# Optimization experiments

Hardware: AMD Instinct MI355X
Metric: run time of the kernel (lower is better)

The kernel has to match this reference:

```python
import jax, jax.numpy as jnp
import numpy as np

MIN_SPAN = 3
MAX_SPAN = 20
LEN_BONUS = 0.01
LN_EPS = 1e-5


def setup_inputs() -> dict:
    key = jax.random.key(0)
    ks = jax.random.split(key, 10)
    B, S, H = 16, 2048, 1024
    D = H // 2
    hidden_states = jax.random.normal(ks[0], (B, S, H), dtype=jnp.float32)
    lengths = jax.random.randint(ks[1], (B,), S // 2, S + 1)
    attention_mask = (jnp.arange(S)[None, :] < lengths[:, None]).astype(jnp.int32)
    return {
        'hidden_states': hidden_states,
        'attention_mask': attention_mask,
        'Wq': 0.02 * jax.random.normal(ks[2], (H, D), dtype=jnp.float32),
        'bq': jnp.zeros((D,), jnp.float32),
        'Wk': 0.02 * jax.random.normal(ks[3], (H, D), dtype=jnp.float32),
        'bk': jnp.zeros((D,), jnp.float32),
        'W1': 0.02 * jax.random.normal(ks[4], (H, D), dtype=jnp.float32),
        'b1': jnp.zeros((D,), jnp.float32),
        'ln_g': jnp.ones((D,), jnp.float32),
        'ln_b': jnp.zeros((D,), jnp.float32),
        'W2': 0.01 * jax.random.normal(ks[5], (D, 1), dtype=jnp.float32),
        'b2': jnp.zeros((1,), jnp.float32),
    }


def _token_scores(hidden_states, mask, Wq, bq, Wk, bk, W1, b1, ln_g, ln_b, W2, b2):
    q = hidden_states @ Wq + bq                      # [B,S,D]
    k = hidden_states @ Wk + bk                      # [B,S,D]
    d = q.shape[-1]
    scores = jnp.einsum('bsd,btd->bst', q, k) / jnp.sqrt(jnp.float32(d))
    scores = jnp.where(mask[:, None, :], scores, -10000.0)
    probs = jax.nn.softmax(scores, axis=-1)
    context = jnp.einsum('bst,bth->bsh', probs, hidden_states)  # [B,S,H]
    h = context @ W1 + b1
    mu = jnp.mean(h, axis=-1, keepdims=True)
    var = jnp.var(h, axis=-1, keepdims=True)
    h = (h - mu) * jax.lax.rsqrt(var + LN_EPS) * ln_g + ln_b
    h = jax.nn.relu(h)                               # dropout: eval mode -> identity
    ts = (h @ W2 + b2)[..., 0]                       # [B,S]
    return jnp.where(mask, ts, -10000.0)


def _rationale_mask(token_scores, mask):
    # Faithful to original: starts[0]==0 always, so prefix subtraction never
    # fires; span score = cumsum[start+L-1]/L + bonus. Argmax over (L asc, start asc)
    # with strict-greater updates == first max of the flattened (L, start) grid.
    B, S = token_scores.shape
    valid_len = jnp.sum(mask, axis=1)                # [B] int
    cum = jnp.cumsum(token_scores, axis=1)           # [B,S]
    L = jnp.arange(MIN_SPAN, MAX_SPAN + 1)           # [NL]
    starts = jnp.arange(S)                           # [S]
    end = jnp.clip(starts[None, :] + L[:, None] - 1, 0, S - 1)   # [NL,S]
    bonus = LEN_BONUS * (L.astype(jnp.float32) / MAX_SPAN)       # [NL]
    grid = cum[:, end] / L[None, :, None].astype(jnp.float32) + bonus[None, :, None]  # [B,NL,S]
    vl = valid_len[:, None, None]
    valid = (L[None, :, None] <= vl) & (starts[None, None, :] <= vl - L[None, :, None])
    grid = jnp.where(valid, grid, -jnp.inf)
    idx = jnp.argmax(grid.reshape(B, -1), axis=1)    # first max -> torch tie-break
    best_L = MIN_SPAN + idx // S
    best_s = idx % S
    pos = jnp.arange(S)[None, :]
    span = (pos >= best_s[:, None]) & (pos < (best_s + best_L)[:, None])
    short = (valid_len <= MIN_SPAN)[:, None]
    short_span = pos < valid_len[:, None]
    return jnp.where(short, short_span, span).astype(token_scores.dtype)


def reference(hidden_states, attention_mask, Wq, bq, Wk, bk, W1, b1, ln_g, ln_b, W2, b2):
    mask = attention_mask.astype(bool)
    token_scores = _token_scores(hidden_states, mask, Wq, bq, Wk, bk, W1, b1, ln_g, ln_b, W2, b2)
    rationale = _rationale_mask(token_scores, mask)
    token_probs = jax.nn.softmax(jnp.where(mask, token_scores, -10000.0), axis=-1)
    attended = hidden_states * rationale[:, :, None]
    lengths = jnp.sum(rationale, axis=1, keepdims=True) + 1e-6
    pooled = jnp.sum(attended, axis=1) / lengths
    return token_scores, rationale, token_probs, attended, pooled
```

## Files before the change

kernel.cpp:

```cpp
#include <hip/hip_runtime.h>

typedef _Float16 f16;
typedef __attribute__((ext_vector_type(8))) _Float16 f16x8;
typedef __attribute__((ext_vector_type(4))) _Float16 f16x4v;
typedef __attribute__((ext_vector_type(4))) float f32x4;

#define B_ 16
#define S_ 2048
#define H_ 1024
#define D_ 512

__device__ __forceinline__ void gload16(const f16* g, f16* l) {
  __builtin_amdgcn_global_load_lds(
      (const __attribute__((address_space(1))) unsigned int*)g,
      (__attribute__((address_space(3))) unsigned int*)l, 16, 0, 0);
}

__global__ __launch_bounds__(256) void cvt_hs_kernel(const float4* __restrict__ in,
                                                     f16x4v* __restrict__ out) {
  long long i = (long long)blockIdx.x * 256 + threadIdx.x;
  float4 v = in[i];
  f16x4v o = {(f16)v.x, (f16)v.y, (f16)v.z, (f16)v.w};
  out[i] = o;
}

__global__ __launch_bounds__(256) void setup_kernel(
    const float* __restrict__ Wq, const float* __restrict__ Wk,
    const float* __restrict__ W1, const float* __restrict__ bq,
    const float* __restrict__ bk, const float* __restrict__ b1,
    const int* __restrict__ mask, f16* __restrict__ Wt,
    float* __restrict__ bias, int* __restrict__ lens) {
  const int blk = blockIdx.x;
  const int tid = threadIdx.x;
  if (blk < 6144) {
    int i = blk * 256 + tid;
    int n = i >> 10;
    int k = i & 1023;
    const float* src = (n < 512) ? Wq : ((n < 1024) ? Wk : W1);
    Wt[i] = (f16)src[k * 512 + (n & 511)];
  } else if (blk < 6150) {
    int i = (blk - 6144) * 256 + tid;
    if (i < 1536) bias[i] = (i < 512) ? bq[i] : ((i < 1024) ? bk[i - 512] : b1[i - 1024]);
  } else {
    int b = blk - 6150;
    int s = 0;
    for (int c = tid; c < S_; c += 256) s += mask[b * S_ + c];
    __shared__ int r[256];
    r[tid] = s;
    __syncthreads();
    for (int o = 128; o > 0; o >>= 1) {
      if (tid < o) r[tid] += r[tid + o];
      __syncthreads();
    }
    if (tid == 0) lens[b] = r[0];
  }
}

template <int MW>
__global__ __launch_bounds__(256, MW) void gemm_bt(
    const f16* __restrict__ A, const f16* __restrict__ Bm, void* __restrict__ Cout,
    void* __restrict__ Cout2,
    int K, int lda, int ldb, int ldc,
    long long sA, long long sB, long long sC,
    float scale, const float* __restrict__ bias, int mode,
    const int* __restrict__ lens, int lflags, int mgrp) {
  const int bz = blockIdx.z;

  const int ntiles = gridDim.x, mtiles = gridDim.y;
  const int flat = blockIdx.y * ntiles + blockIdx.x;
  const int per = mgrp * ntiles;
  const int grp = flat / per;
  const int rem = flat - grp * per;
  const int gbase = grp * mgrp;
  int gsz = mtiles - gbase;
  if (gsz > mgrp) gsz = mgrp;
  const int mt = gbase + rem % gsz;
  const int nt = rem / gsz;
  const int m0 = mt * 128;
  const int n0 = nt * 128;

  int Keff = K;
  if (lflags) {
    const int len = lens[(lflags & 1) ? (m0 >> 11) : bz];
    if ((lflags & 3) && (m0 & 2047) >= len) return;
    if ((lflags & 4) && n0 >= len) return;
    if (lflags & 8) { int kl = (len + 63) & ~63; Keff = kl < K ? kl : K; }
  }

  A += (long long)bz * sA;
  Bm += (long long)bz * sB;

  __shared__ f16 As[128 * 64];
  __shared__ f16 Bs[128 * 64];

  const int tid = threadIdx.x;
  const int lane = tid & 63;
  const int wid = tid >> 6;
  const int wm = wid & 1, wn = wid >> 1;

  f32x4 acc[4][4] = {};

  const int lr8 = lane >> 3;
  const int sg = lane & 7;

  for (int k0 = 0; k0 < Keff; k0 += 64) {
#pragma unroll
    for (int it = 0; it < 4; ++it) {
      const int r0 = it * 32 + wid * 8;
      const int r = r0 + lr8;
      const int cg = sg ^ (r & 7);
      gload16(A + (long long)(m0 + r) * lda + k0 + cg * 8, As + r0 * 64);
      gload16(Bm + (long long)(n0 + r) * ldb + k0 + cg * 8, Bs + r0 * 64);
    }
    __syncthreads();

#pragma unroll
    for (int kk = 0; kk < 64; kk += 32) {
      const int cg = (kk >> 3) + (lane >> 4);
      f16x8 af[4], bf[4];
#pragma unroll
      for (int i = 0; i < 4; ++i) {
        const int row = wm * 64 + i * 16 + (lane & 15);
        af[i] = *(const f16x8*)(As + row * 64 + ((cg ^ (row & 7)) << 3));
      }
#pragma unroll
      for (int j = 0; j < 4; ++j) {
        const int row = wn * 64 + j * 16 + (lane & 15);
        bf[j] = *(const f16x8*)(Bs + row * 64 + ((cg ^ (row & 7)) << 3));
      }
#pragma unroll
      for (int i = 0; i < 4; ++i)
#pragma unroll
        for (int j = 0; j < 4; ++j)
          acc[i][j] = __builtin_amdgcn_mfma_f32_16x16x32_f16(af[i], bf[j], acc[i][j], 0, 0, 0);
    }
    __syncthreads();
  }

  const long long cb = (long long)bz * sC;
  const int lr = ((lane >> 4) << 2);
  const int lc = lane & 15;
#pragma unroll
  for (int i = 0; i < 4; ++i) {
#pragma unroll
    for (int j = 0; j < 4; ++j) {
      const int col = n0 + wn * 64 + j * 16 + lc;
      const float bv = bias ? bias[col] : 0.0f;
      if (mode == 2 || (mode == 3 && col >= 1024)) {
        const int rowb = m0 + wm * 64 + i * 16 + lr;
        const int b = rowb >> 11, t = rowb & 2047;
        const int d = (mode == 3) ? (col - 1024) : col;
        f16* dst = (f16*)((mode == 3) ? Cout2 : Cout);
        f16x4v pk;
#pragma unroll
        for (int r = 0; r < 4; ++r) pk[r] = (f16)(acc[i][j][r] * scale + bv);
        *(f16x4v*)(dst + ((long long)b << 20) + (long long)d * 2048 + t) = pk;
      } else {
#pragma unroll
        for (int r = 0; r < 4; ++r) {
          const int row = m0 + wm * 64 + i * 16 + lr + r;
          float v = acc[i][j][r] * scale + bv;
          if (mode == 0)
            ((float*)Cout)[cb + (long long)row * ldc + col] = v;
          else
            ((f16*)Cout)[cb + (long long)row * ldc + col] = (f16)v;
        }
      }
    }
  }
}

__global__ __launch_bounds__(256) void softmax_rows_kernel(f16* __restrict__ sc,
                                                           const int* __restrict__ lens) {
  const int tid = threadIdx.x;
  const int lane = tid & 63;
  const int row = blockIdx.x * 4 + (tid >> 6);
  const int len = lens[row >> 11];
  const int cl = (len + 127) & ~127;
  if ((row & 2047) >= cl) return;
  f16* p = sc + (long long)row * S_;

  f16x8 v[4];
#pragma unroll
  for (int c = 0; c < 4; ++c)
    if (c * 512 < cl) v[c] = *(const f16x8*)(p + c * 512 + lane * 8);

  float m = -1e30f;
#pragma unroll
  for (int c = 0; c < 4; ++c) {
    if (c * 512 >= cl) continue;
#pragma unroll
    for (int j = 0; j < 8; ++j) {
      const int col = c * 512 + lane * 8 + j;
      if (col < len) m = fmaxf(m, (float)v[c][j]);
    }
  }
#pragma unroll
  for (int o = 32; o > 0; o >>= 1) m = fmaxf(m, __shfl_xor(m, o, 64));

  float e[32];
  float s = 0.0f;
#pragma unroll
  for (int c = 0; c < 4; ++c) {
    if (c * 512 >= cl) continue;
#pragma unroll
    for (int j = 0; j < 8; ++j) {
      const int col = c * 512 + lane * 8 + j;
      const float x = (col < len) ? __expf((float)v[c][j] - m) : 0.0f;
      e[c * 8 + j] = x;
      s += x;
    }
  }
#pragma unroll
  for (int o = 32; o > 0; o >>= 1) s += __shfl_xor(s, o, 64);
  const float inv = 1.0f / s;

#pragma unroll
  for (int c = 0; c < 4; ++c) {
    if (c * 512 >= cl) continue;
    f16x8 w;
#pragma unroll
    for (int j = 0; j < 8; ++j) w[j] = (f16)(e[c * 8 + j] * inv);
    *(f16x8*)(p + c * 512 + lane * 8) = w;
  }
}

__global__ __launch_bounds__(256) void ln_score_kernel(
    const float* __restrict__ h, const int* __restrict__ lens,
    const float* __restrict__ g, const float* __restrict__ bt,
    const float* __restrict__ W2, const float* __restrict__ b2,
    float* __restrict__ ts, float* __restrict__ out_ts) {
  const int token = blockIdx.x;
  const int tid = threadIdx.x;
  const int b = token >> 11, s = token & (S_ - 1);
  if (s >= lens[b]) {
    if (tid == 0) { ts[token] = -10000.0f; out_ts[token] = -10000.0f; }
    return;
  }
  const float* hp = h + (long long)token * D_;
  float x0 = hp[tid], x1 = hp[tid + 256];
  __shared__ float r1[256], r2[256];
  r1[tid] = x0 + x1;
  r2[tid] = x0 * x0 + x1 * x1;
  __syncthreads();
  for (int o = 128; o > 0; o >>= 1) {
    if (tid < o) { r1[tid] += r1[tid + o]; r2[tid] += r2[tid + o]; }
    __syncthreads();
  }
  const float mu = r1[0] * (1.0f / D_);
  const float var = r2[0] * (1.0f / D_) - mu * mu;
  const float rs = rsqrtf(var + 1e-5f);
  float y0 = fmaxf((x0 - mu) * rs * g[tid] + bt[tid], 0.0f);
  float y1 = fmaxf((x1 - mu) * rs * g[tid + 256] + bt[tid + 256], 0.0f);
  float d = y0 * W2[tid] + y1 * W2[tid + 256];
  __syncthreads();
  r1[tid] = d;
  __syncthreads();
  for (int o = 128; o > 0; o >>= 1) {
    if (tid < o) r1[tid] += r1[tid + o];
    __syncthreads();
  }
  if (tid == 0) {
    float v = r1[0] + b2[0];
    ts[token] = v;
    out_ts[token] = v;
  }
}

__global__ __launch_bounds__(256) void rationale_kernel(
    const float* __restrict__ ts, const int* __restrict__ lens,
    float* __restrict__ out_rat, int* __restrict__ span) {
  const int b = blockIdx.x;
  const int tid = threadIdx.x;
  const int len = lens[b];
  __shared__ float cum[S_];
  __shared__ float rbest[256];
  __shared__ int ridx[256];

  for (int s = tid; s < S_; s += 256)
    cum[s] = (s < len) ? ts[b * S_ + s] : -10000.0f;
  __syncthreads();
  if (tid == 0) {
    float a = 0.0f;
    for (int s = 0; s < S_; s += 4) {
      float4 v = *(float4*)(cum + s);
      a += v.x; v.x = a;
      a += v.y; v.y = a;
      a += v.z; v.z = a;
      a += v.w; v.w = a;
      *(float4*)(cum + s) = v;
    }
  }
  __syncthreads();

  float best = -3.4e38f;
  int bidx = 0x7fffffff;
  for (int idx = tid; idx < 18 * S_; idx += 256) {
    const int l = idx >> 11;
    const int s = idx & (S_ - 1);
    const int L = l + 3;
    if (L <= len && s <= len - L) {
      const float gv = cum[s + L - 1] / (float)L + 0.01f * ((float)L / 20.0f);
      if (gv > best) { best = gv; bidx = idx; }
    }
  }
  rbest[tid] = best;
  ridx[tid] = bidx;
  __syncthreads();
  for (int o = 128; o > 0; o >>= 1) {
    if (tid < o) {
      if (rbest[tid + o] > rbest[tid] ||
          (rbest[tid + o] == rbest[tid] && ridx[tid + o] < ridx[tid])) {
        rbest[tid] = rbest[tid + o];
        ridx[tid] = ridx[tid + o];
      }
    }
    __syncthreads();
  }
  const int bi = ridx[0];
  int start, sl;
  if (len <= 3) { start = 0; sl = len; }
  else { start = bi & (S_ - 1); sl = (bi >> 11) + 3; }
  if (tid == 0) { span[2 * b] = start; span[2 * b + 1] = sl; }
  for (int s = tid; s < S_; s += 256)
    out_rat[b * S_ + s] = (s >= start && s < start + sl) ? 1.0f : 0.0f;
}

__global__ __launch_bounds__(256) void tprobs_kernel(const float* __restrict__ ts,
                                                     const int* __restrict__ lens,
                                                     float* __restrict__ out) {
  const int b = blockIdx.x;
  const int tid = threadIdx.x;
  const int len = lens[b];
  const float* p = ts + b * S_;
  __shared__ float r[256];
  float m = -1e30f;
  for (int c = tid; c < len; c += 256) m = fmaxf(m, p[c]);
  r[tid] = m;
  __syncthreads();
  for (int o = 128; o > 0; o >>= 1) {
    if (tid < o) r[tid] = fmaxf(r[tid], r[tid + o]);
    __syncthreads();
  }
  m = r[0];
  __syncthreads();
  float s = 0.0f;
  for (int c = tid; c < len; c += 256) s += expf(p[c] - m);
  r[tid] = s;
  __syncthreads();
  for (int o = 128; o > 0; o >>= 1) {
    if (tid < o) r[tid] += r[tid + o];
    __syncthreads();
  }
  const float inv = 1.0f / r[0];
  for (int c = tid; c < S_; c += 256)
    out[b * S_ + c] = (c < len) ? expf(p[c] - m) * inv : 0.0f;
}

__global__ __launch_bounds__(256) void attended_kernel(const float4* __restrict__ hs,
                                                       const int* __restrict__ span,
                                                       float4* __restrict__ out) {
  long long i = (long long)blockIdx.x * 256 + threadIdx.x;
  const int token = (int)(i >> 8);
  const int b = token >> 11;
  const int s = token & (S_ - 1);
  const int st = span[2 * b], ln = span[2 * b + 1];
  float4 v = {0.0f, 0.0f, 0.0f, 0.0f};
  if (s >= st && s < st + ln) v = hs[i];
  out[i] = v;
}

__global__ __launch_bounds__(256) void pooled_kernel(const float* __restrict__ hs,
                                                     const int* __restrict__ span,
                                                     float* __restrict__ out) {
  const int b = blockIdx.x;
  const int tid = threadIdx.x;
  const int st = span[2 * b], ln = span[2 * b + 1];
  const float inv = 1.0f / ((float)ln + 1e-6f);
  for (int h = tid; h < H_; h += 256) {
    float s = 0.0f;
    for (int t = st; t < st + ln; ++t)
      s += hs[(long long)(b * S_ + t) * H_ + h];
    out[b * H_ + h] = s * inv;
  }
}

extern "C" void kernel_launch(void* const* d_in, const int* in_sizes, int n_in,
                              void* d_out, int out_size, void* d_ws, size_t ws_size,
                              hipStream_t stream) {
  const float* hs = (const float*)d_in[0];
  const int* amask = (const int*)d_in[1];
  const float* Wq = (const float*)d_in[2];
  const float* bq = (const float*)d_in[3];
  const float* Wk = (const float*)d_in[4];
  const float* bk = (const float*)d_in[5];
  const float* W1 = (const float*)d_in[6];
  const float* b1 = (const float*)d_in[7];
  const float* ln_g = (const float*)d_in[8];
  const float* ln_b = (const float*)d_in[9];
  const float* W2 = (const float*)d_in[10];
  const float* b2 = (const float*)d_in[11];

  float* out = (float*)d_out;
  char* ws = (char*)d_ws;

  const long long off_hs16 = 0;
  const long long off_qk = 67108864;
  const long long off_vt = 134217728;
  const long long off_wt = 167772160;
  const long long off_bias = 170917888;
  const long long off_ts = 170926080;
  const long long off_lens = 171057152;
  const long long off_span = 171057216;
  const long long off_scores = 171057408;

  f16* hs16 = (f16*)(ws + off_hs16);
  float* hbuf = (float*)(ws + off_hs16);
  f16* qk16 = (f16*)(ws + off_qk);
  f16* vt = (f16*)(ws + off_vt);
  f16* Wt = (f16*)(ws + off_wt);
  float* bias_full = (float*)(ws + off_bias);
  float* ts = (float*)(ws + off_ts);
  int* lens = (int*)(ws + off_lens);
  int* span = (int*)(ws + off_span);
  f16* scores = (f16*)(ws + off_scores);

  const long long SC_PER_B = (long long)S_ * S_ * 2;
  int nb = 16;
  while (nb > 1 && off_scores + (long long)nb * SC_PER_B > (long long)ws_size) nb >>= 1;

  float* out_ts = out;
  float* out_rat = out + 32768;
  float* out_tp = out + 65536;
  float4* out_att = (float4*)(out + 98304);
  float* out_pool = out + 33652736;

  setup_kernel<<<dim3(6166), dim3(256), 0, stream>>>(Wq, Wk, W1, bq, bk, b1, amask,
                                                     Wt, bias_full, lens);
  cvt_hs_kernel<<<dim3(32768), dim3(256), 0, stream>>>((const float4*)hs, (f16x4v*)hs16);

  gemm_bt<2><<<dim3(12, 256, 1), dim3(256), 0, stream>>>(
      hs16, Wt, (void*)qk16, (void*)vt, 1024, 1024, 1024, 1024,
      0LL, 0LL, 0LL, 1.0f, bias_full, 3, lens, 1, 8);

  const int chunks = 16 / nb;
  for (int c = 0; c < chunks; ++c) {
    const int b0 = c * nb;
    gemm_bt<4><<<dim3(16, 16, nb), dim3(256), 0, stream>>>(
        qk16 + (long long)b0 * S_ * 1024,
        qk16 + (long long)b0 * S_ * 1024 + 512,
        (void*)scores, (void*)nullptr, 512, 1024, 1024, 2048,
        (long long)S_ * 1024, (long long)S_ * 1024, (long long)S_ * S_,
        0.044194173824159216f , (const float*)nullptr, 1,
        lens + b0, 2 | 4, 8);
    softmax_rows_kernel<<<dim3(nb * S_ / 4), dim3(256), 0, stream>>>(scores, lens + b0);
    gemm_bt<4><<<dim3(4, 16, nb), dim3(256), 0, stream>>>(
        scores, vt + ((long long)b0 << 20),
        (void*)(hbuf + (long long)b0 * S_ * D_), (void*)nullptr, 2048, 2048, 2048, 512,
        (long long)S_ * S_, 1LL << 20, (long long)S_ * D_,
        1.0f, (const float*)nullptr, 0, lens + b0, 2 | 8, 1);
  }

  ln_score_kernel<<<dim3(B_ * S_), dim3(256), 0, stream>>>(hbuf, lens, ln_g, ln_b,
                                                           W2, b2, ts, out_ts);
  rationale_kernel<<<dim3(B_), dim3(256), 0, stream>>>(ts, lens, out_rat, span);
  tprobs_kernel<<<dim3(B_), dim3(256), 0, stream>>>(ts, lens, out_tp);
  attended_kernel<<<dim3(32768), dim3(256), 0, stream>>>((const float4*)hs, span, out_att);
  pooled_kernel<<<dim3(B_), dim3(256), 0, stream>>>(hs, span, out_pool);
}
```

Measured before the change: 667.6 us.

## Merge setup/convert, tail kernels; warp-per-token layernorm; skip masked token conversion

Fuses the fp16 conversion of hidden states into the setup kernel and skips converting tokens whose mask is zero. Rewrites the layernorm-score kernel so one 64-lane wavefront handles one token, using vector loads and shuffle reductions in place of shared-memory tree reductions. Also merges the rationale and token-probability kernels, and the attended and pooled kernels, to cut launch count. Skipping masked tokens leaves their fp16 rows uninitialised, which relies on downstream GEMMs ignoring rows past each sequence length.

```diff
diff --git a/kernel.cpp b/kernel.cpp
--- a/kernel.cpp
+++ b/kernel.cpp
@@ -16,33 +16,32 @@
       (__attribute__((address_space(3))) unsigned int*)l, 16, 0, 0);
 }
 
-__global__ __launch_bounds__(256) void cvt_hs_kernel(const float4* __restrict__ in,
-                                                     f16x4v* __restrict__ out) {
-  long long i = (long long)blockIdx.x * 256 + threadIdx.x;
-  float4 v = in[i];
-  f16x4v o = {(f16)v.x, (f16)v.y, (f16)v.z, (f16)v.w};
-  out[i] = o;
-}
-
-__global__ __launch_bounds__(256) void setup_kernel(
+__global__ __launch_bounds__(256) void setup_cvt_kernel(
+    const float4* __restrict__ hs4, const int* __restrict__ mask,
     const float* __restrict__ Wq, const float* __restrict__ Wk,
     const float* __restrict__ W1, const float* __restrict__ bq,
     const float* __restrict__ bk, const float* __restrict__ b1,
-    const int* __restrict__ mask, f16* __restrict__ Wt,
+    f16x4v* __restrict__ hs16, f16* __restrict__ Wt,
     float* __restrict__ bias, int* __restrict__ lens) {
   const int blk = blockIdx.x;
   const int tid = threadIdx.x;
-  if (blk < 6144) {
-    int i = blk * 256 + tid;
+  if (blk < 32768) {
+    if (mask[blk] == 0) return;
+    long long i = (long long)blk * 256 + tid;
+    float4 v = hs4[i];
+    f16x4v o = {(f16)v.x, (f16)v.y, (f16)v.z, (f16)v.w};
+    hs16[i] = o;
+  } else if (blk < 32768 + 6144) {
+    int i = (blk - 32768) * 256 + tid;
     int n = i >> 10;
     int k = i & 1023;
     const float* src = (n < 512) ? Wq : ((n < 1024) ? Wk : W1);
     Wt[i] = (f16)src[k * 512 + (n & 511)];
-  } else if (blk < 6150) {
-    int i = (blk - 6144) * 256 + tid;
+  } else if (blk < 32768 + 6150) {
+    int i = (blk - 32768 - 6144) * 256 + tid;
     if (i < 1536) bias[i] = (i < 512) ? bq[i] : ((i < 1024) ? bk[i - 512] : b1[i - 1024]);
   } else {
-    int b = blk - 6150;
+    int b = blk - 32768 - 6150;
     int s = 0;
     for (int c = tid; c < S_; c += 256) s += mask[b * S_ + c];
     __shared__ int r[256];
@@ -230,46 +229,54 @@
     const float* __restrict__ g, const float* __restrict__ bt,
     const float* __restrict__ W2, const float* __restrict__ b2,
     float* __restrict__ ts, float* __restrict__ out_ts) {
-  const int token = blockIdx.x;
-  const int tid = threadIdx.x;
+  const int tid = threadIdx.x;
+  const int lane = tid & 63;
+  const int token = blockIdx.x * 4 + (tid >> 6);
   const int b = token >> 11, s = token & (S_ - 1);
   if (s >= lens[b]) {
-    if (tid == 0) { ts[token] = -10000.0f; out_ts[token] = -10000.0f; }
+    if (lane == 0) { ts[token] = -10000.0f; out_ts[token] = -10000.0f; }
     return;
   }
   const float* hp = h + (long long)token * D_;
-  float x0 = hp[tid], x1 = hp[tid + 256];
-  __shared__ float r1[256], r2[256];
-  r1[tid] = x0 + x1;
-  r2[tid] = x0 * x0 + x1 * x1;
-  __syncthreads();
-  for (int o = 128; o > 0; o >>= 1) {
-    if (tid < o) { r1[tid] += r1[tid + o]; r2[tid] += r2[tid + o]; }
-    __syncthreads();
-  }
-  const float mu = r1[0] * (1.0f / D_);
-  const float var = r2[0] * (1.0f / D_) - mu * mu;
+  const int o8 = lane * 8;
+  float4 xa = *(const float4*)(hp + o8);
+  float4 xb = *(const float4*)(hp + o8 + 4);
+  float s1 = xa.x + xa.y + xa.z + xa.w + xb.x + xb.y + xb.z + xb.w;
+  float s2 = xa.x * xa.x + xa.y * xa.y + xa.z * xa.z + xa.w * xa.w +
+             xb.x * xb.x + xb.y * xb.y + xb.z * xb.z + xb.w * xb.w;
+#pragma unroll
+  for (int o = 32; o > 0; o >>= 1) {
+    s1 += __shfl_xor(s1, o, 64);
+    s2 += __shfl_xor(s2, o, 64);
+  }
+  const float mu = s1 * (1.0f / D_);
+  const float var = s2 * (1.0f / D_) - mu * mu;
   const float rs = rsqrtf(var + 1e-5f);
-  float y0 = fmaxf((x0 - mu) * rs * g[tid] + bt[tid], 0.0f);
-  float y1 = fmaxf((x1 - mu) * rs * g[tid + 256] + bt[tid + 256], 0.0f);
-  float d = y0 * W2[tid] + y1 * W2[tid + 256];
-  __syncthreads();
-  r1[tid] = d;
-  __syncthreads();
-  for (int o = 128; o > 0; o >>= 1) {
-    if (tid < o) r1[tid] += r1[tid + o];
-    __syncthreads();
-  }
-  if (tid == 0) {
-    float v = r1[0] + b2[0];
+  float4 ga = *(const float4*)(g + o8), gb = *(const float4*)(g + o8 + 4);
+  float4 ba = *(const float4*)(bt + o8), bb = *(const float4*)(bt + o8 + 4);
+  float4 wa = *(const float4*)(W2 + o8), wb = *(const float4*)(W2 + o8 + 4);
+  float d = 0.0f;
+  d += fmaxf((xa.x - mu) * rs * ga.x + ba.x, 0.0f) * wa.x;
+  d += fmaxf((xa.y - mu) * rs * ga.y + ba.y, 0.0f) * wa.y;
+  d += fmaxf((xa.z - mu) * rs * ga.z + ba.z, 0.0f) * wa.z;
+  d += fmaxf((xa.w - mu) * rs * ga.w + ba.w, 0.0f) * wa.w;
+  d += fmaxf((xb.x - mu) * rs * gb.x + bb.x, 0.0f) * wb.x;
+  d += fmaxf((xb.y - mu) * rs * gb.y + bb.y, 0.0f) * wb.y;
+  d += fmaxf((xb.z - mu) * rs * gb.z + bb.z, 0.0f) * wb.z;
+  d += fmaxf((xb.w - mu) * rs * gb.w + bb.w, 0.0f) * wb.w;
+#pragma unroll
+  for (int o = 32; o > 0; o >>= 1) d += __shfl_xor(d, o, 64);
+  if (lane == 0) {
+    float v = d + b2[0];
     ts[token] = v;
     out_ts[token] = v;
   }
 }
 
-__global__ __launch_bounds__(256) void rationale_kernel(
+__global__ __launch_bounds__(256) void rat_tprobs_kernel(
     const float* __restrict__ ts, const int* __restrict__ lens,
-    float* __restrict__ out_rat, int* __restrict__ span) {
+    float* __restrict__ out_rat, float* __restrict__ out_tp,
+    int* __restrict__ span) {
   const int b = blockIdx.x;
   const int tid = threadIdx.x;
   const int len = lens[b];
@@ -324,64 +331,57 @@
   if (tid == 0) { span[2 * b] = start; span[2 * b + 1] = sl; }
   for (int s = tid; s < S_; s += 256)
     out_rat[b * S_ + s] = (s >= start && s < start + sl) ? 1.0f : 0.0f;
-}
-
-__global__ __launch_bounds__(256) void tprobs_kernel(const float* __restrict__ ts,
-                                                     const int* __restrict__ lens,
-                                                     float* __restrict__ out) {
-  const int b = blockIdx.x;
-  const int tid = threadIdx.x;
-  const int len = lens[b];
+
+  __syncthreads();
   const float* p = ts + b * S_;
-  __shared__ float r[256];
   float m = -1e30f;
   for (int c = tid; c < len; c += 256) m = fmaxf(m, p[c]);
-  r[tid] = m;
+  rbest[tid] = m;
   __syncthreads();
   for (int o = 128; o > 0; o >>= 1) {
-    if (tid < o) r[tid] = fmaxf(r[tid], r[tid + o]);
-    __syncthreads();
-  }
-  m = r[0];
-  __syncthreads();
-  float s = 0.0f;
-  for (int c = tid; c < len; c += 256) s += expf(p[c] - m);
-  r[tid] = s;
+    if (tid < o) rbest[tid] = fmaxf(rbest[tid], rbest[tid + o]);
+    __syncthreads();
+  }
+  m = rbest[0];
+  __syncthreads();
+  float sm = 0.0f;
+  for (int c = tid; c < len; c += 256) sm += expf(p[c] - m);
+  rbest[tid] = sm;
   __syncthreads();
   for (int o = 128; o > 0; o >>= 1) {
-    if (tid < o) r[tid] += r[tid + o];
-    __syncthreads();
-  }
-  const float inv = 1.0f / r[0];
+    if (tid < o) rbest[tid] += rbest[tid + o];
+    __syncthreads();
+  }
+  const float inv = 1.0f / rbest[0];
   for (int c = tid; c < S_; c += 256)
-    out[b * S_ + c] = (c < len) ? expf(p[c] - m) * inv : 0.0f;
-}
-
-__global__ __launch_bounds__(256) void attended_kernel(const float4* __restrict__ hs,
-                                                       const int* __restrict__ span,
-                                                       float4* __restrict__ out) {
-  long long i = (long long)blockIdx.x * 256 + threadIdx.x;
-  const int token = (int)(i >> 8);
-  const int b = token >> 11;
-  const int s = token & (S_ - 1);
-  const int st = span[2 * b], ln = span[2 * b + 1];
-  float4 v = {0.0f, 0.0f, 0.0f, 0.0f};
-  if (s >= st && s < st + ln) v = hs[i];
-  out[i] = v;
-}
-
-__global__ __launch_bounds__(256) void pooled_kernel(const float* __restrict__ hs,
-                                                     const int* __restrict__ span,
-                                                     float* __restrict__ out) {
-  const int b = blockIdx.x;
-  const int tid = threadIdx.x;
-  const int st = span[2 * b], ln = span[2 * b + 1];
-  const float inv = 1.0f / ((float)ln + 1e-6f);
-  for (int h = tid; h < H_; h += 256) {
-    float s = 0.0f;
-    for (int t = st; t < st + ln; ++t)
-      s += hs[(long long)(b * S_ + t) * H_ + h];
-    out[b * H_ + h] = s * inv;
+    out_tp[b * S_ + c] = (c < len) ? expf(p[c] - m) * inv : 0.0f;
+}
+
+__global__ __launch_bounds__(256) void att_pool_kernel(
+    const float4* __restrict__ hs4, const float* __restrict__ hs,
+    const int* __restrict__ span, float4* __restrict__ out_att,
+    float* __restrict__ out_pool) {
+  const int blk = blockIdx.x;
+  const int tid = threadIdx.x;
+  if (blk < 32768) {
+    long long i = (long long)blk * 256 + tid;
+    const int token = (int)(i >> 8);
+    const int b = token >> 11;
+    const int s = token & (S_ - 1);
+    const int st = span[2 * b], ln = span[2 * b + 1];
+    float4 v = {0.0f, 0.0f, 0.0f, 0.0f};
+    if (s >= st && s < st + ln) v = hs4[i];
+    out_att[i] = v;
+  } else {
+    const int b = blk - 32768;
+    const int st = span[2 * b], ln = span[2 * b + 1];
+    const float inv = 1.0f / ((float)ln + 1e-6f);
+    for (int h = tid; h < H_; h += 256) {
+      float s = 0.0f;
+      for (int t = st; t < st + ln; ++t)
+        s += hs[(long long)(b * S_ + t) * H_ + h];
+      out_pool[b * H_ + h] = s * inv;
+    }
   }
 }
 
@@ -435,9 +435,9 @@
   float4* out_att = (float4*)(out + 98304);
   float* out_pool = out + 33652736;
 
-  setup_kernel<<<dim3(6166), dim3(256), 0, stream>>>(Wq, Wk, W1, bq, bk, b1, amask,
-                                                     Wt, bias_full, lens);
-  cvt_hs_kernel<<<dim3(32768), dim3(256), 0, stream>>>((const float4*)hs, (f16x4v*)hs16);
+  setup_cvt_kernel<<<dim3(32768 + 6144 + 6 + 16), dim3(256), 0, stream>>>(
+      (const float4*)hs, amask, Wq, Wk, W1, bq, bk, b1,
+      (f16x4v*)hs16, Wt, bias_full, lens);
 
   gemm_bt<2><<<dim3(12, 256, 1), dim3(256), 0, stream>>>(
       hs16, Wt, (void*)qk16, (void*)vt, 1024, 1024, 1024, 1024,
@@ -461,10 +461,9 @@
         1.0f, (const float*)nullptr, 0, lens + b0, 2 | 8, 1);
   }
 
-  ln_score_kernel<<<dim3(B_ * S_), dim3(256), 0, stream>>>(hbuf, lens, ln_g, ln_b,
-                                                           W2, b2, ts, out_ts);
-  rationale_kernel<<<dim3(B_), dim3(256), 0, stream>>>(ts, lens, out_rat, span);
-  tprobs_kernel<<<dim3(B_), dim3(256), 0, stream>>>(ts, lens, out_tp);
-  attended_kernel<<<dim3(32768), dim3(256), 0, stream>>>((const float4*)hs, span, out_att);
-  pooled_kernel<<<dim3(B_), dim3(256), 0, stream>>>(hs, span, out_pool);
-}
+  ln_score_kernel<<<dim3(B_ * S_ / 4), dim3(256), 0, stream>>>(hbuf, lens, ln_g, ln_b,
+                                                               W2, b2, ts, out_ts);
+  rat_tprobs_kernel<<<dim3(B_), dim3(256), 0, stream>>>(ts, lens, out_rat, out_tp, span);
+  att_pool_kernel<<<dim3(32768 + 16), dim3(256), 0, stream>>>(
+      (const float4*)hs, hs, span, out_att, out_pool);
+}
```

New measurement: 634.2 us. -5.0%, faster.
